# Optimization experiments

Measured on AMD Instinct MI355X. Metric: run time of the kernel, lower is better.

## Reference

```python
import jax, jax.numpy as jnp
import numpy as np

B, C, D, H, W = 4, 256, 16, 16, 16


def setup_inputs() -> dict:
    key = jax.random.key(0)
    ks = jax.random.split(key, 9)
    s = 1.0 / np.sqrt(C)
    inp = {
        "x": jax.random.normal(ks[0], (B, C, D, H, W), dtype=jnp.float32),
        "wq": jax.random.normal(ks[1], (C, C), dtype=jnp.float32) * s,
        "bq": jax.random.normal(ks[2], (C,), dtype=jnp.float32) * 0.02,
        "wk": jax.random.normal(ks[3], (C, C), dtype=jnp.float32) * s,
        "bk": jax.random.normal(ks[4], (C,), dtype=jnp.float32) * 0.02,
        "wv": jax.random.normal(ks[5], (C, C), dtype=jnp.float32) * s,
        "bv": jax.random.normal(ks[6], (C,), dtype=jnp.float32) * 0.02,
        "wp": jax.random.normal(ks[7], (C, C), dtype=jnp.float32) * s,
        "bp": jax.random.normal(ks[8], (C,), dtype=jnp.float32) * 0.02,
    }
    return inp


def reference(x, wq, bq, wk, bk, wv, bv, wp, bp):
    b, c, d, h, w = x.shape
    xf = x.reshape(b, c, d * h * w)  # (B, C, N)
    # 1x1 Conv3d == per-voxel linear map over channels
    q = jnp.einsum('oc,bcn->bon', wq, xf) + bq[:, None]
    k = jnp.einsum('oc,bcn->bon', wk, xf) + bk[:, None]
    v = jnp.einsum('oc,bcn->bon', wv, xf) + bv[:, None]
    # scores[b,i,j] = q[:, :, i] . k[:, :, j], scaled AFTER the bmm (as in source)
    scores = jnp.einsum('bci,bcj->bij', q, k) * (c ** -0.5)
    p = jax.nn.softmax(scores, axis=2)  # (B, N, N), softmax over keys j
    # attention[b,c,i] = sum_j v[b,c,j] * p[b,i,j]
    attn = jnp.einsum('bcj,bij->bci', v, p)
    out = jnp.einsum('oc,bcn->bon', wp, attn) + bp[:, None]
    return x + out.reshape(b, c, d, h, w)
```

## Files before the change

kernel.cpp:

```cpp
#include <hip/hip_runtime.h>

typedef unsigned short u16;
typedef unsigned int u32;
typedef __bf16 v8bf __attribute__((ext_vector_type(8)));
typedef float v4f __attribute__((ext_vector_type(4)));

#define DEV __device__ __forceinline__

constexpr int CB = 4;
constexpr int C = 256;
constexpr int NN = 4096;
constexpr float LOG2E = 1.4426950408889634f;

DEV u16 f2bf(float f) {
  union { float f; u32 u; } v; v.f = f;
  u32 r = v.u + 0x7fffu + ((v.u >> 16) & 1u);
  return (u16)(r >> 16);
}
DEV float bf2f(u16 h) {
  union { u32 u; float f; } v; v.u = ((u32)h) << 16; return v.f;
}

DEV void dma16(const u16* g, const u16* lds_base) {
  __builtin_amdgcn_global_load_lds(
      (const __attribute__((address_space(1))) void*)(unsigned long long)g,
      (__attribute__((address_space(3))) void*)(u32)(unsigned long long)lds_base,
      16, 0, 0);
}

__global__ __launch_bounds__(256) void k_transpose(const float* __restrict__ x,
                                                   u16* __restrict__ xT) {
  __shared__ float tile[32][33];
  int b = blockIdx.z;
  int n0 = blockIdx.x * 32, c0 = blockIdx.y * 32;
  int tx = threadIdx.x & 31, ty = threadIdx.x >> 5;
  const float* xb = x + (long)b * C * NN;
#pragma unroll
  for (int r = 0; r < 4; ++r)
    tile[ty + r * 8][tx] = xb[(long)(c0 + ty + r * 8) * NN + n0 + tx];
  __syncthreads();
  u16* xTb = xT + (long)b * NN * C;
#pragma unroll
  for (int r = 0; r < 4; ++r)
    xTb[(long)(n0 + ty + r * 8) * C + c0 + tx] = f2bf(tile[tx][ty + r * 8]);
}

__global__ __launch_bounds__(256) void k_cvt4(const float* __restrict__ s0,
                                              const float* __restrict__ s1,
                                              const float* __restrict__ s2,
                                              const float* __restrict__ s3,
                                              u16* __restrict__ d0, u16* __restrict__ d1,
                                              u16* __restrict__ d2, u16* __restrict__ d3,
                                              float* __restrict__ Mbuf) {
  if (blockIdx.x == 0 && blockIdx.y == 0 && threadIdx.x < 8) Mbuf[threadIdx.x] = 0.f;
  int wsel = blockIdx.y;
  const float* s = wsel == 0 ? s0 : wsel == 1 ? s1 : wsel == 2 ? s2 : s3;
  u16* d = wsel == 0 ? d0 : wsel == 1 ? d1 : wsel == 2 ? d2 : d3;
  int i = blockIdx.x * 256 + threadIdx.x;
  d[i] = f2bf(s[i]);
}

DEV void stage_tile(const u16* __restrict__ g, u16* lds, int t) {
#pragma unroll
  for (int i = 0; i < 8; ++i) {
    int id = t + i * 256;
    int row = id >> 5, ch = id & 31;
    *reinterpret_cast<float4*>(lds + row * 264 + ch * 8) =
        *reinterpret_cast<const float4*>(g + row * 256 + ch * 8);
  }
}

__global__ __launch_bounds__(256) void k_qkv(
    const u16* __restrict__ xT, const u16* __restrict__ wqb, const u16* __restrict__ wkb,
    const u16* __restrict__ wvb, const float* __restrict__ bq, const float* __restrict__ bk,
    const float* __restrict__ bv, u16* __restrict__ qO, u16* __restrict__ kO,
    u16* __restrict__ vO) {
  __shared__ __align__(16) u16 Ash[64 * 264];
  __shared__ __align__(16) u16 Bsh[64 * 264];
  int t = threadIdx.x, w = t >> 6, lane = t & 63, lr = lane & 15, q = lane >> 4;
  int m0 = blockIdx.x * 64, n0 = blockIdx.y * 64, b = blockIdx.z;
  stage_tile(xT + (long)b * NN * C + (long)m0 * 256, Ash, t);
#pragma unroll 1
  for (int wsel = 0; wsel < 3; ++wsel) {
    const u16* wptr = wsel == 0 ? wqb : wsel == 1 ? wkb : wvb;
    stage_tile(wptr + (long)n0 * 256, Bsh, t);
    __syncthreads();
    v4f acc[4];
#pragma unroll
    for (int nt = 0; nt < 4; ++nt)
#pragma unroll
      for (int r = 0; r < 4; ++r) acc[nt][r] = 0.f;
#pragma unroll
    for (int ks = 0; ks < 8; ++ks) {
      v8bf a = *reinterpret_cast<const v8bf*>(Ash + (w * 16 + lr) * 264 + ks * 32 + q * 8);
#pragma unroll
      for (int nt = 0; nt < 4; ++nt) {
        v8bf bb = *reinterpret_cast<const v8bf*>(Bsh + (nt * 16 + lr) * 264 + ks * 32 + q * 8);
        acc[nt] = __builtin_amdgcn_mfma_f32_16x16x32_bf16(a, bb, acc[nt], 0, 0, 0);
      }
    }
    const float* bias = wsel == 0 ? bq : wsel == 1 ? bk : bv;
#pragma unroll
    for (int nt = 0; nt < 4; ++nt) {
#pragma unroll
      for (int r = 0; r < 4; ++r) {
        int gm = m0 + w * 16 + q * 4 + r;
        int gn = n0 + nt * 16 + lr;
        float val = acc[nt][r] + bias[gn];
        if (wsel == 0) {
          qO[((long)b * NN + gm) * C + gn] = f2bf(val * (0.0625f * LOG2E));
        } else if (wsel == 1) {
          kO[((long)b * NN + gm) * C + gn] = f2bf(val);
        } else {
          vO[(long)b * C * NN + (long)gn * NN + gm] = f2bf(val);
        }
      }
    }
    __syncthreads();
  }
}

__global__ __launch_bounds__(256) void k_maxnorm(const u16* __restrict__ qT,
                                                 const u16* __restrict__ kT,
                                                 float* __restrict__ Mbuf) {
  int b = blockIdx.z, tsel = blockIdx.y;
  const u16* src = (tsel ? kT : qT) + (long)b * NN * C;
  int row = blockIdx.x * 64 + (threadIdx.x >> 2);
  const uint4* pp =
      reinterpret_cast<const uint4*>(src + (long)row * C + (threadIdx.x & 3) * 64);
  float s = 0.f;
#pragma unroll
  for (int u = 0; u < 8; ++u) {
    uint4 d = pp[u];
    const u16* e = reinterpret_cast<const u16*>(&d);
#pragma unroll
    for (int i = 0; i < 8; ++i) { float f = bf2f(e[i]); s += f * f; }
  }
  s += __shfl_xor(s, 1, 64);
  s += __shfl_xor(s, 2, 64);
#pragma unroll
  for (int d2 = 4; d2 < 64; d2 <<= 1) s = fmaxf(s, __shfl_xor(s, d2, 64));
  if ((threadIdx.x & 63) == 0)
    atomicMax((u32*)(Mbuf + tsel * 4 + b), __float_as_uint(s));
}

__global__ __launch_bounds__(256) void k_gemm(
    const u16* __restrict__ A, long aStr, const u16* __restrict__ Bm, long bStr,
    const float* __restrict__ biasM, const float* __restrict__ biasN,
    const float* __restrict__ resid, long rStr, float scale,
    float* __restrict__ outF, u16* __restrict__ outH, long oStr, int ldm, int ldn) {
  __shared__ __align__(16) u16 Ash[64 * 264];
  __shared__ __align__(16) u16 Bsh[64 * 264];
  int t = threadIdx.x;
  int w = t >> 6, lane = t & 63, lr = lane & 15, q = lane >> 4;
  int m0 = blockIdx.x * 64, n0 = blockIdx.y * 64, b = blockIdx.z;
  stage_tile(A + b * aStr + (long)m0 * 256, Ash, t);
  stage_tile(Bm + b * bStr + (long)n0 * 256, Bsh, t);
  __syncthreads();
  v4f acc[4];
#pragma unroll
  for (int nt = 0; nt < 4; ++nt)
#pragma unroll
    for (int r = 0; r < 4; ++r) acc[nt][r] = 0.f;
#pragma unroll
  for (int ks = 0; ks < 8; ++ks) {
    v8bf a = *reinterpret_cast<const v8bf*>(Ash + (w * 16 + lr) * 264 + ks * 32 + q * 8);
#pragma unroll
    for (int nt = 0; nt < 4; ++nt) {
      v8bf bb = *reinterpret_cast<const v8bf*>(Bsh + (nt * 16 + lr) * 264 + ks * 32 + q * 8);
      acc[nt] = __builtin_amdgcn_mfma_f32_16x16x32_bf16(a, bb, acc[nt], 0, 0, 0);
    }
  }
#pragma unroll
  for (int nt = 0; nt < 4; ++nt) {
#pragma unroll
    for (int r = 0; r < 4; ++r) {
      int gm = m0 + w * 16 + q * 4 + r;
      int gn = n0 + nt * 16 + lr;
      float val = acc[nt][r];
      if (biasM) val += biasM[gm];
      if (biasN) val += biasN[gn];
      val *= scale;
      long addr = b * oStr + (long)gm * ldm + (long)gn * ldn;
      if (resid) val += resid[b * rStr + (long)gm * ldm + (long)gn * ldn];
      if (outF) outF[addr] = val;
      else outH[addr] = f2bf(val);
    }
  }
}

DEV void flash_issue(const u16* kb, const u16* vb, const u16* kshb, const u16* vshb,
                     int j0, int w, int lane) {
#pragma unroll
  for (int i = 0; i < 4; ++i) {
    int idx = w * 4 + i;
    int kr = idx * 2 + (lane >> 5);
    int kc = (lane & 31) ^ (kr & 7);
    dma16(kb + (long)(j0 + kr) * 256 + kc * 8, kshb + idx * 512);
  }
#pragma unroll
  for (int i = 0; i < 4; ++i) {
    int idx = w * 4 + i;
    int vr = idx * 16 + (lane >> 2);
    int vc = (lane & 3) ^ ((vr ^ (vr >> 2)) & 3);
    dma16(vb + (long)vr * NN + j0 + vc * 8, vshb + idx * 512);
  }
}

__global__ __launch_bounds__(256, 2) void k_flash(const u16* __restrict__ qT,
                                                  const u16* __restrict__ kT,
                                                  const u16* __restrict__ V,
                                                  u16* __restrict__ op0,
                                                  u16* __restrict__ op1,
                                                  u16* __restrict__ op2,
                                                  u16* __restrict__ op3,
                                                  float* __restrict__ ml,
                                                  const float* __restrict__ Mbuf,
                                                  int span) {
  __shared__ __align__(16) u16 ksh[2][32 * 256];
  __shared__ __align__(16) u16 vsh[2][256 * 32];
  __shared__ __align__(16) u16 psh[4 * 16 * 40];
  int t = threadIdx.x;
  int w = t >> 6, lane = t & 63, lr = lane & 15, q = lane >> 4;
  int b = blockIdx.z, h = blockIdx.y;
  int i0 = blockIdx.x * 64;
  const u16* qb = qT + ((long)b * NN + i0 + w * 16) * C;
  const u16* kb = kT + (long)b * NN * C;
  const u16* vb = V + (long)b * C * NN;
  float M = sqrtf(Mbuf[b] * Mbuf[4 + b]) + 1.0f;

  v8bf qf[8];
#pragma unroll
  for (int ks = 0; ks < 8; ++ks)
    qf[ks] = *reinterpret_cast<const v8bf*>(qb + lr * C + ks * 32 + q * 8);

  v4f accO[16];
#pragma unroll
  for (int ct = 0; ct < 16; ++ct)
#pragma unroll
    for (int r = 0; r < 4; ++r) accO[ct][r] = 0.f;
  float lsum[4] = {0.f, 0.f, 0.f, 0.f};

  u16* pw = psh + w * 640;
  const int xk = lr & 7;
  const int xv = (lr ^ (lr >> 2)) & 3;

  int jstart = h * span;
  int niter = span >> 5;
  flash_issue(kb, vb, ksh[0], vsh[0], jstart, w, lane);
  int cur = 0;
#pragma unroll 1
  for (int it = 0; it < niter; ++it) {
    int j0 = jstart + (it << 5);
    int jn = (it + 1 < niter) ? j0 + 32 : jstart;
    asm volatile("s_waitcnt lgkmcnt(0)\n\ts_barrier" ::: "memory");
    flash_issue(kb, vb, ksh[cur ^ 1], vsh[cur ^ 1], jn, w, lane);
    asm volatile("s_waitcnt vmcnt(8)\n\ts_barrier" ::: "memory");

    const u16* kcur = ksh[cur];
    const u16* vcur = vsh[cur];
    v4f s[2];
#pragma unroll
    for (int jt = 0; jt < 2; ++jt)
#pragma unroll
      for (int r = 0; r < 4; ++r) s[jt][r] = 0.f;
#pragma unroll
    for (int ks = 0; ks < 8; ++ks) {
#pragma unroll
      for (int jt = 0; jt < 2; ++jt) {
        v8bf kf = *reinterpret_cast<const v8bf*>(
            kcur + (jt * 16 + lr) * 256 + (((ks * 4 + q) ^ xk) << 3));
        s[jt] = __builtin_amdgcn_mfma_f32_16x16x32_bf16(qf[ks], kf, s[jt], 0, 0, 0);
      }
    }

#pragma unroll
    for (int jt = 0; jt < 2; ++jt) {
#pragma unroll
      for (int r = 0; r < 4; ++r) {
        float p = exp2f(s[jt][r] - M);
        lsum[r] += p;
        u32 pb = (__float_as_uint(p) + 0x8000u) >> 16;
        pw[(q * 4 + r) * 40 + jt * 16 + lr] = (u16)pb;
      }
    }
    asm volatile("s_waitcnt lgkmcnt(0)" ::: "memory");
    v8bf pa = *reinterpret_cast<const v8bf*>(pw + lr * 40 + q * 8);
#pragma unroll
    for (int ct = 0; ct < 16; ++ct) {
      v8bf v0 = *reinterpret_cast<const v8bf*>(
          vcur + (ct * 16 + lr) * 32 + ((q ^ xv) << 3));
      accO[ct] = __builtin_amdgcn_mfma_f32_16x16x32_bf16(pa, v0, accO[ct], 0, 0, 0);
    }
    cur ^= 1;
  }

#pragma unroll
  for (int r = 0; r < 4; ++r) {
#pragma unroll
    for (int d = 1; d < 16; d <<= 1) lsum[r] += __shfl_xor(lsum[r], d, 64);
  }
  float inv[4];
#pragma unroll
  for (int r = 0; r < 4; ++r) inv[r] = 1.0f / lsum[r];
  u16* opp = h == 0 ? op0 : h == 1 ? op1 : h == 2 ? op2 : op3;
  u16* ob = opp + ((long)b * NN + i0 + w * 16) * C;
#pragma unroll
  for (int ct = 0; ct < 16; ++ct)
#pragma unroll
    for (int r = 0; r < 4; ++r)
      ob[(q * 4 + r) * C + ct * 16 + lr] = f2bf(accO[ct][r] * inv[r]);
  if (lr == 0) {
    long rbase = ((long)h * CB + b) * NN + i0 + w * 16 + q * 4;
#pragma unroll
    for (int r = 0; r < 4; ++r) {
      ml[(rbase + r) * 2] = M;
      ml[(rbase + r) * 2 + 1] = lsum[r];
    }
  }
}

__global__ __launch_bounds__(256) void k_combine(const u16* __restrict__ p0,
                                                 const u16* __restrict__ p1,
                                                 const u16* __restrict__ p2,
                                                 const u16* __restrict__ p3,
                                                 const float* __restrict__ ml,
                                                 u16* __restrict__ o, int js) {
  long row = (long)blockIdx.x * 8 + (threadIdx.x >> 5);
  int tc = (threadIdx.x & 31) * 8;
  float m[4], l[4];
  float mx = -3.0e38f;
  for (int h = 0; h < js; ++h) {
    m[h] = ml[((long)h * CB * NN + row) * 2];
    l[h] = ml[((long)h * CB * NN + row) * 2 + 1];
    mx = fmaxf(mx, m[h]);
  }
  float tot = 0.f, a[4];
  for (int h = 0; h < js; ++h) { a[h] = exp2f(m[h] - mx) * l[h]; tot += a[h]; }
  float inv = 1.f / tot;
  float acc[8];
#pragma unroll
  for (int i = 0; i < 8; ++i) acc[i] = 0.f;
  const u16* ps[4] = {p0, p1, p2, p3};
  for (int h = 0; h < js; ++h) {
    uint4 u = *reinterpret_cast<const uint4*>(ps[h] + row * C + tc);
    const u16* p = reinterpret_cast<const u16*>(&u);
    float wgt = a[h] * inv;
#pragma unroll
    for (int i = 0; i < 8; ++i) acc[i] += wgt * bf2f(p[i]);
  }
  u16 outv[8];
#pragma unroll
  for (int i = 0; i < 8; ++i) outv[i] = f2bf(acc[i]);
  *reinterpret_cast<uint4*>(o + row * C + tc) = *reinterpret_cast<const uint4*>(outv);
}

extern "C" void kernel_launch(void* const* d_in, const int* in_sizes, int n_in,
                              void* d_out, int out_size, void* d_ws, size_t ws_size,
                              hipStream_t stream) {
  const float* x = (const float*)d_in[0];
  const float* wq = (const float*)d_in[1];
  const float* bq = (const float*)d_in[2];
  const float* wk = (const float*)d_in[3];
  const float* bk = (const float*)d_in[4];
  const float* wv = (const float*)d_in[5];
  const float* bv = (const float*)d_in[6];
  const float* wp = (const float*)d_in[7];
  const float* bp = (const float*)d_in[8];
  float* out = (float*)d_out;
  char* ws = (char*)d_ws;

  const long SLOT = 8388608L;
  const size_t NEED4 = 524288UL + 7 * 8388608UL + 524288UL + 4096UL;
  int js = (ws_size >= NEED4) ? 4 : 2;

  u16* wqb = (u16*)(ws + 0);
  u16* wkb = (u16*)(ws + 131072L);
  u16* wvb = (u16*)(ws + 262144L);
  u16* wpb = (u16*)(ws + 393216L);
  char* base = ws + 524288L;
  u16* xT  = (u16*)(base);
  u16* qTw = (u16*)(base + 1 * SLOT);
  u16* kTw = (u16*)(base + 2 * SLOT);
  u16* vw  = (u16*)(base + 3 * SLOT);
  u16* op1 = (u16*)(base + 4 * SLOT);
  u16* op2 = js == 4 ? (u16*)(base + 5 * SLOT) : op1;
  u16* op3 = js == 4 ? (u16*)(base + 6 * SLOT) : op1;
  float* ml = (float*)(base + (js == 4 ? 7 : 5) * SLOT);
  float* Mbuf = ml + 131072;
  u16* op0 = xT;
  u16* oW  = qTw;

  k_cvt4<<<dim3(256, 4), 256, 0, stream>>>(wq, wk, wv, wp, wqb, wkb, wvb, wpb, Mbuf);
  k_transpose<<<dim3(128, 8, CB), 256, 0, stream>>>(x, xT);
  k_qkv<<<dim3(64, 4, CB), 256, 0, stream>>>(xT, wqb, wkb, wvb, bq, bk, bv, qTw, kTw, vw);
  k_maxnorm<<<dim3(64, 2, CB), 256, 0, stream>>>(qTw, kTw, Mbuf);
  k_flash<<<dim3(64, js, CB), 256, 0, stream>>>(qTw, kTw, vw, op0, op1, op2, op3, ml,
                                                Mbuf, NN / js);
  k_combine<<<2048, 256, 0, stream>>>(op0, op1, op2, op3, ml, oW, js);

  long nc = (long)NN * C;
  k_gemm<<<dim3(4, 64, CB), 256, 0, stream>>>(wpb, 0, oW, nc, bp, nullptr, x, nc,
                                              1.0f, out, nullptr, nc, NN, 1);
}
```

Before: 274.4 us.

## Process 32 query rows per wave in flash kernel to reuse K/V tiles

Result: slower. 314.2 us (+14.5%).

```diff
diff --git a/kernel.cpp b/kernel.cpp
--- a/kernel.cpp
+++ b/kernel.cpp
@@ -219,29 +219,32 @@
                                                   int span) {
   __shared__ __align__(16) u16 ksh[2][32 * 256];
   __shared__ __align__(16) u16 vsh[2][256 * 32];
-  __shared__ __align__(16) u16 psh[4 * 16 * 40];
+  __shared__ __align__(16) u16 psh[4 * 2 * 16 * 40];
   int t = threadIdx.x;
   int w = t >> 6, lane = t & 63, lr = lane & 15, q = lane >> 4;
   int b = blockIdx.z, h = blockIdx.y;
-  int i0 = blockIdx.x * 64;
-  const u16* qb = qT + ((long)b * NN + i0 + w * 16) * C;
+  int i0 = blockIdx.x * 128;
+  const u16* qb = qT + ((long)b * NN + i0 + w * 32) * C;
   const u16* kb = kT + (long)b * NN * C;
   const u16* vb = V + (long)b * C * NN;
   float M = sqrtf(Mbuf[b] * Mbuf[4 + b]) + 1.0f;
 
-  v8bf qf[8];
-#pragma unroll
-  for (int ks = 0; ks < 8; ++ks)
-    qf[ks] = *reinterpret_cast<const v8bf*>(qb + lr * C + ks * 32 + q * 8);
-
-  v4f accO[16];
+  v8bf qf0[8], qf1[8];
+#pragma unroll
+  for (int ks = 0; ks < 8; ++ks) {
+    qf0[ks] = *reinterpret_cast<const v8bf*>(qb + lr * C + ks * 32 + q * 8);
+    qf1[ks] = *reinterpret_cast<const v8bf*>(qb + (16 + lr) * C + ks * 32 + q * 8);
+  }
+
+  v4f accO0[16], accO1[16];
 #pragma unroll
   for (int ct = 0; ct < 16; ++ct)
 #pragma unroll
-    for (int r = 0; r < 4; ++r) accO[ct][r] = 0.f;
-  float lsum[4] = {0.f, 0.f, 0.f, 0.f};
-
-  u16* pw = psh + w * 640;
+    for (int r = 0; r < 4; ++r) { accO0[ct][r] = 0.f; accO1[ct][r] = 0.f; }
+  float lsum0[4] = {0.f, 0.f, 0.f, 0.f};
+  float lsum1[4] = {0.f, 0.f, 0.f, 0.f};
+
+  u16* pw = psh + w * 1280;
   const int xk = lr & 7;
   const int xv = (lr ^ (lr >> 2)) & 3;
 
@@ -251,26 +254,26 @@
   int cur = 0;
 #pragma unroll 1
   for (int it = 0; it < niter; ++it) {
-    int j0 = jstart + (it << 5);
-    int jn = (it + 1 < niter) ? j0 + 32 : jstart;
+    int jn = (it + 1 < niter) ? jstart + ((it + 1) << 5) : jstart;
     asm volatile("s_waitcnt lgkmcnt(0)\n\ts_barrier" ::: "memory");
     flash_issue(kb, vb, ksh[cur ^ 1], vsh[cur ^ 1], jn, w, lane);
     asm volatile("s_waitcnt vmcnt(8)\n\ts_barrier" ::: "memory");
 
     const u16* kcur = ksh[cur];
     const u16* vcur = vsh[cur];
-    v4f s[2];
+    v4f s0[2], s1[2];
 #pragma unroll
     for (int jt = 0; jt < 2; ++jt)
 #pragma unroll
-      for (int r = 0; r < 4; ++r) s[jt][r] = 0.f;
+      for (int r = 0; r < 4; ++r) { s0[jt][r] = 0.f; s1[jt][r] = 0.f; }
 #pragma unroll
     for (int ks = 0; ks < 8; ++ks) {
 #pragma unroll
       for (int jt = 0; jt < 2; ++jt) {
         v8bf kf = *reinterpret_cast<const v8bf*>(
             kcur + (jt * 16 + lr) * 256 + (((ks * 4 + q) ^ xk) << 3));
-        s[jt] = __builtin_amdgcn_mfma_f32_16x16x32_bf16(qf[ks], kf, s[jt], 0, 0, 0);
+        s0[jt] = __builtin_amdgcn_mfma_f32_16x16x32_bf16(qf0[ks], kf, s0[jt], 0, 0, 0);
+        s1[jt] = __builtin_amdgcn_mfma_f32_16x16x32_bf16(qf1[ks], kf, s1[jt], 0, 0, 0);
       }
     }
 
@@ -278,19 +281,25 @@
     for (int jt = 0; jt < 2; ++jt) {
 #pragma unroll
       for (int r = 0; r < 4; ++r) {
-        float p = exp2f(s[jt][r] - M);
-        lsum[r] += p;
-        u32 pb = (__float_as_uint(p) + 0x8000u) >> 16;
-        pw[(q * 4 + r) * 40 + jt * 16 + lr] = (u16)pb;
+        float p0 = exp2f(s0[jt][r] - M);
+        float p1 = exp2f(s1[jt][r] - M);
+        lsum0[r] += p0;
+        lsum1[r] += p1;
+        u32 pb0 = (__float_as_uint(p0) + 0x8000u) >> 16;
+        u32 pb1 = (__float_as_uint(p1) + 0x8000u) >> 16;
+        pw[(q * 4 + r) * 40 + jt * 16 + lr] = (u16)pb0;
+        pw[640 + (q * 4 + r) * 40 + jt * 16 + lr] = (u16)pb1;
       }
     }
     asm volatile("s_waitcnt lgkmcnt(0)" ::: "memory");
-    v8bf pa = *reinterpret_cast<const v8bf*>(pw + lr * 40 + q * 8);
+    v8bf pa0 = *reinterpret_cast<const v8bf*>(pw + lr * 40 + q * 8);
+    v8bf pa1 = *reinterpret_cast<const v8bf*>(pw + 640 + lr * 40 + q * 8);
 #pragma unroll
     for (int ct = 0; ct < 16; ++ct) {
       v8bf v0 = *reinterpret_cast<const v8bf*>(
           vcur + (ct * 16 + lr) * 32 + ((q ^ xv) << 3));
-      accO[ct] = __builtin_amdgcn_mfma_f32_16x16x32_bf16(pa, v0, accO[ct], 0, 0, 0);
+      accO0[ct] = __builtin_amdgcn_mfma_f32_16x16x32_bf16(pa0, v0, accO0[ct], 0, 0, 0);
+      accO1[ct] = __builtin_amdgcn_mfma_f32_16x16x32_bf16(pa1, v0, accO1[ct], 0, 0, 0);
     }
     cur ^= 1;
   }
@@ -298,24 +307,31 @@
 #pragma unroll
   for (int r = 0; r < 4; ++r) {
 #pragma unroll
-    for (int d = 1; d < 16; d <<= 1) lsum[r] += __shfl_xor(lsum[r], d, 64);
-  }
-  float inv[4];
-#pragma unroll
-  for (int r = 0; r < 4; ++r) inv[r] = 1.0f / lsum[r];
+    for (int d = 1; d < 16; d <<= 1) {
+      lsum0[r] += __shfl_xor(lsum0[r], d, 64);
+      lsum1[r] += __shfl_xor(lsum1[r], d, 64);
+    }
+  }
+  float inv0[4], inv1[4];
+#pragma unroll
+  for (int r = 0; r < 4; ++r) { inv0[r] = 1.0f / lsum0[r]; inv1[r] = 1.0f / lsum1[r]; }
   u16* opp = h == 0 ? op0 : h == 1 ? op1 : h == 2 ? op2 : op3;
-  u16* ob = opp + ((long)b * NN + i0 + w * 16) * C;
+  u16* ob = opp + ((long)b * NN + i0 + w * 32) * C;
 #pragma unroll
   for (int ct = 0; ct < 16; ++ct)
 #pragma unroll
-    for (int r = 0; r < 4; ++r)
-      ob[(q * 4 + r) * C + ct * 16 + lr] = f2bf(accO[ct][r] * inv[r]);
+    for (int r = 0; r < 4; ++r) {
+      ob[(q * 4 + r) * C + ct * 16 + lr] = f2bf(accO0[ct][r] * inv0[r]);
+      ob[(16 + q * 4 + r) * C + ct * 16 + lr] = f2bf(accO1[ct][r] * inv1[r]);
+    }
   if (lr == 0) {
-    long rbase = ((long)h * CB + b) * NN + i0 + w * 16 + q * 4;
+    long rbase = ((long)h * CB + b) * NN + i0 + w * 32 + q * 4;
 #pragma unroll
     for (int r = 0; r < 4; ++r) {
       ml[(rbase + r) * 2] = M;
-      ml[(rbase + r) * 2 + 1] = lsum[r];
+      ml[(rbase + r) * 2 + 1] = lsum0[r];
+      ml[(rbase + 16 + r) * 2] = M;
+      ml[(rbase + 16 + r) * 2 + 1] = lsum1[r];
     }
   }
 }
@@ -395,7 +411,7 @@
   k_transpose<<<dim3(128, 8, CB), 256, 0, stream>>>(x, xT);
   k_qkv<<<dim3(64, 4, CB), 256, 0, stream>>>(xT, wqb, wkb, wvb, bq, bk, bv, qTw, kTw, vw);
   k_maxnorm<<<dim3(64, 2, CB), 256, 0, stream>>>(qTw, kTw, Mbuf);
-  k_flash<<<dim3(64, js, CB), 256, 0, stream>>>(qTw, kTw, vw, op0, op1, op2, op3, ml,
+  k_flash<<<dim3(32, js, CB), 256, 0, stream>>>(qTw, kTw, vw, op0, op1, op2, op3, ml,
                                                 Mbuf, NN / js);
   k_combine<<<2048, 256, 0, stream>>>(op0, op1, op2, op3, ml, oW, js);
 
```

## Stage GEMM tiles via direct global-to-LDS DMA with XOR swizzle

Applied to the files above, without the earlier changes.

After: 274.1 us. No clear change (-0.1%).

```diff
diff --git a/kernel.cpp b/kernel.cpp
--- a/kernel.cpp
+++ b/kernel.cpp
@@ -60,13 +60,13 @@
   d[i] = f2bf(s[i]);
 }
 
-DEV void stage_tile(const u16* __restrict__ g, u16* lds, int t) {
+DEV void stage_dma(const u16* __restrict__ g, const u16* lds, int w, int lane) {
 #pragma unroll
   for (int i = 0; i < 8; ++i) {
-    int id = t + i * 256;
-    int row = id >> 5, ch = id & 31;
-    *reinterpret_cast<float4*>(lds + row * 264 + ch * 8) =
-        *reinterpret_cast<const float4*>(g + row * 256 + ch * 8);
+    int idx = w * 8 + i;
+    int r = idx * 2 + (lane >> 5);
+    int cg = (lane & 31) ^ (r & 7);
+    dma16(g + (long)r * 256 + cg * 8, lds + idx * 512);
   }
 }
 
@@ -75,16 +75,16 @@
     const u16* __restrict__ wvb, const float* __restrict__ bq, const float* __restrict__ bk,
     const float* __restrict__ bv, u16* __restrict__ qO, u16* __restrict__ kO,
     u16* __restrict__ vO) {
-  __shared__ __align__(16) u16 Ash[64 * 264];
-  __shared__ __align__(16) u16 Bsh[64 * 264];
+  __shared__ __align__(16) u16 Ash[64 * 256];
+  __shared__ __align__(16) u16 Bsh[64 * 256];
   int t = threadIdx.x, w = t >> 6, lane = t & 63, lr = lane & 15, q = lane >> 4;
   int m0 = blockIdx.x * 64, n0 = blockIdx.y * 64, b = blockIdx.z;
-  stage_tile(xT + (long)b * NN * C + (long)m0 * 256, Ash, t);
+  const int xk = lr & 7;
+  stage_dma(xT + (long)b * NN * C + (long)m0 * 256, Ash, w, lane);
+  stage_dma(wqb + (long)n0 * 256, Bsh, w, lane);
+  asm volatile("s_waitcnt vmcnt(0)\n\ts_barrier" ::: "memory");
 #pragma unroll 1
   for (int wsel = 0; wsel < 3; ++wsel) {
-    const u16* wptr = wsel == 0 ? wqb : wsel == 1 ? wkb : wvb;
-    stage_tile(wptr + (long)n0 * 256, Bsh, t);
-    __syncthreads();
     v4f acc[4];
 #pragma unroll
     for (int nt = 0; nt < 4; ++nt)
@@ -92,13 +92,17 @@
       for (int r = 0; r < 4; ++r) acc[nt][r] = 0.f;
 #pragma unroll
     for (int ks = 0; ks < 8; ++ks) {
-      v8bf a = *reinterpret_cast<const v8bf*>(Ash + (w * 16 + lr) * 264 + ks * 32 + q * 8);
+      int cg = ((ks * 4 + q) ^ xk) << 3;
+      v8bf a = *reinterpret_cast<const v8bf*>(Ash + (w * 16 + lr) * 256 + cg);
 #pragma unroll
       for (int nt = 0; nt < 4; ++nt) {
-        v8bf bb = *reinterpret_cast<const v8bf*>(Bsh + (nt * 16 + lr) * 264 + ks * 32 + q * 8);
+        v8bf bb = *reinterpret_cast<const v8bf*>(Bsh + (nt * 16 + lr) * 256 + cg);
         acc[nt] = __builtin_amdgcn_mfma_f32_16x16x32_bf16(a, bb, acc[nt], 0, 0, 0);
       }
     }
+    asm volatile("s_waitcnt lgkmcnt(0)\n\ts_barrier" ::: "memory");
+    if (wsel < 2)
+      stage_dma((wsel == 0 ? wkb : wvb) + (long)n0 * 256, Bsh, w, lane);
     const float* bias = wsel == 0 ? bq : wsel == 1 ? bk : bv;
 #pragma unroll
     for (int nt = 0; nt < 4; ++nt) {
@@ -116,7 +120,7 @@
         }
       }
     }
-    __syncthreads();
+    asm volatile("s_waitcnt vmcnt(0)\n\ts_barrier" ::: "memory");
   }
 }
 
@@ -149,14 +153,15 @@
     const float* __restrict__ biasM, const float* __restrict__ biasN,
     const float* __restrict__ resid, long rStr, float scale,
     float* __restrict__ outF, u16* __restrict__ outH, long oStr, int ldm, int ldn) {
-  __shared__ __align__(16) u16 Ash[64 * 264];
-  __shared__ __align__(16) u16 Bsh[64 * 264];
+  __shared__ __align__(16) u16 Ash[64 * 256];
+  __shared__ __align__(16) u16 Bsh[64 * 256];
   int t = threadIdx.x;
   int w = t >> 6, lane = t & 63, lr = lane & 15, q = lane >> 4;
   int m0 = blockIdx.x * 64, n0 = blockIdx.y * 64, b = blockIdx.z;
-  stage_tile(A + b * aStr + (long)m0 * 256, Ash, t);
-  stage_tile(Bm + b * bStr + (long)n0 * 256, Bsh, t);
-  __syncthreads();
+  const int xk = lr & 7;
+  stage_dma(A + b * aStr + (long)m0 * 256, Ash, w, lane);
+  stage_dma(Bm + b * bStr + (long)n0 * 256, Bsh, w, lane);
+  asm volatile("s_waitcnt vmcnt(0)\n\ts_barrier" ::: "memory");
   v4f acc[4];
 #pragma unroll
   for (int nt = 0; nt < 4; ++nt)
@@ -164,10 +169,11 @@
     for (int r = 0; r < 4; ++r) acc[nt][r] = 0.f;
 #pragma unroll
   for (int ks = 0; ks < 8; ++ks) {
-    v8bf a = *reinterpret_cast<const v8bf*>(Ash + (w * 16 + lr) * 264 + ks * 32 + q * 8);
+    int cg = ((ks * 4 + q) ^ xk) << 3;
+    v8bf a = *reinterpret_cast<const v8bf*>(Ash + (w * 16 + lr) * 256 + cg);
 #pragma unroll
     for (int nt = 0; nt < 4; ++nt) {
-      v8bf bb = *reinterpret_cast<const v8bf*>(Bsh + (nt * 16 + lr) * 264 + ks * 32 + q * 8);
+      v8bf bb = *reinterpret_cast<const v8bf*>(Bsh + (nt * 16 + lr) * 256 + cg);
       acc[nt] = __builtin_amdgcn_mfma_f32_16x16x32_bf16(a, bb, acc[nt], 0, 0, 0);
     }
   }
```
